# Performance work log

Measured on AMD Instinct MI355X. Metric: run time of the kernel, lower is better.

## Reference

```python
import jax, jax.numpy as jnp
import numpy as np

N_ATOMS = 100_000   # atom_node.size(0)
N_EDGES = 3_200_000  # avg degree 32


def setup_inputs() -> dict:
    key = jax.random.key(0)
    k1, k2, k3, k4, k5 = jax.random.split(key, 5)
    disp = jax.random.normal(k1, (N_EDGES, 3), dtype=jnp.float32)
    a = jax.random.normal(k2, (N_EDGES,), dtype=jnp.float32)
    b = jax.random.normal(k3, (N_EDGES,), dtype=jnp.float32)
    edge_index = jax.random.randint(k4, (2, N_EDGES), 0, N_ATOMS, dtype=jnp.int64)
    atom_node = jax.random.randint(k5, (N_ATOMS,), 0, 100, dtype=jnp.int64)
    return {"disp": disp, "a": a, "b": b, "edge_index": edge_index, "atom_node": atom_node}


def _energy(disp, a, b):
    # surrogate differentiable per-edge energy: E = sum_e a_e*r2_e + b_e*exp(-r2_e)
    r2 = jnp.sum(disp * disp, axis=-1)  # [E]
    return jnp.sum(a * r2 + b * jnp.exp(-r2))


def reference(disp, a, b, edge_index, atom_node):
    n = atom_node.shape[0]
    # force = -dE/d(disp), create_graph analog: jax grads are differentiable
    force_edge = -jax.grad(_energy, argnums=0)(disp, a, b)  # [E,3]
    # dual scatter-add over the two endpoint index rows, then subtract
    f_src = jax.ops.segment_sum(force_edge, edge_index[0], num_segments=n)  # [N,3]
    f_dst = jax.ops.segment_sum(force_edge, edge_index[1], num_segments=n)  # [N,3]
    return f_src - f_dst
```

## Files before the change

kernel.cpp:

```cpp
#include <hip/hip_runtime.h>
#include <hip/hip_bf16.h>
#include <hip/hip_fp16.h>
#include <math.h>
#include <stdint.h>

constexpr int TPB         = 256;
constexpr int U           = 4;
constexpr int ROUND_EDGES = TPB * U;
constexpr int ROUND_REC   = ROUND_EDGES * 2;
constexpr int EPB         = 2048;
constexpr int NPB_SHIFT   = 10;
constexpr int NODES_PER_B = 1 << NPB_SHIFT;
constexpr int NB_MAX      = 128;
constexpr int CAP         = 56;
constexpr int SPLIT       = 8;
constexpr int OCAP        = 262144;

__device__ __forceinline__ uint64_t pack_rec(int local, float fx, float fy, float fz) {
    uint64_t hx = __half_as_ushort(__float2half(fx));
    uint64_t hy = __half_as_ushort(__float2half(fy));
    uint64_t hz = __half_as_ushort(__float2half(fz));
    return (uint64_t)(unsigned)local | (hx << 16) | (hy << 32) | (hz << 48);
}

__global__ void __launch_bounds__(TPB)
p1_partition(const float* __restrict__ disp,
             const float* __restrict__ a,
             const float* __restrict__ b,
             const int* __restrict__ src,
             const int* __restrict__ dst,
             uint64_t* __restrict__ grecords,
             int* __restrict__ gcnt,
             uint4* __restrict__ ovf,
             int* __restrict__ ovf_cnt,
             int E, int NB, int NBLK) {
    __shared__ int      s_cnt[NB_MAX];
    __shared__ int      s_off[NB_MAX];
    __shared__ int      s_gd[NB_MAX];
    __shared__ uint64_t s_rec[ROUND_REC];
    __shared__ uint8_t  s_bin[ROUND_REC];

    const int t = threadIdx.x;
    const int blk = blockIdx.x;
    const int base = blk * EPB;
    const int bend = min(base + EPB, E);

    int wcur = 0;

    for (int rb = base; rb < bend; rb += ROUND_EDGES) {
        const int rend = min(rb + ROUND_EDGES, bend);
        if (t < NB_MAX) s_cnt[t] = 0;
        __syncthreads();

        const int e0 = rb + t * U;
        float dxv[U], dyv[U], dzv[U], av[U], bv[U];
        int sv[U], dv[U];
        bool valid[U];
        if (e0 + U <= rend) {
            const float4* p = (const float4*)(disp + (size_t)3 * e0);
            float4 q0 = p[0], q1 = p[1], q2 = p[2];
            dxv[0] = q0.x; dyv[0] = q0.y; dzv[0] = q0.z;
            dxv[1] = q0.w; dyv[1] = q1.x; dzv[1] = q1.y;
            dxv[2] = q1.z; dyv[2] = q1.w; dzv[2] = q2.x;
            dxv[3] = q2.y; dyv[3] = q2.z; dzv[3] = q2.w;
            float4 qa = *(const float4*)(a + e0);
            av[0] = qa.x; av[1] = qa.y; av[2] = qa.z; av[3] = qa.w;
            float4 qb = *(const float4*)(b + e0);
            bv[0] = qb.x; bv[1] = qb.y; bv[2] = qb.z; bv[3] = qb.w;
            int4 qs = *(const int4*)(src + e0);
            sv[0] = qs.x; sv[1] = qs.y; sv[2] = qs.z; sv[3] = qs.w;
            int4 qd = *(const int4*)(dst + e0);
            dv[0] = qd.x; dv[1] = qd.y; dv[2] = qd.z; dv[3] = qd.w;
#pragma unroll
            for (int u = 0; u < U; ++u) valid[u] = true;
        } else {
#pragma unroll
            for (int u = 0; u < U; ++u) {
                int e = e0 + u;
                valid[u] = (e < rend);
                if (valid[u]) {
                    dxv[u] = disp[3 * e + 0];
                    dyv[u] = disp[3 * e + 1];
                    dzv[u] = disp[3 * e + 2];
                    av[u] = a[e]; bv[u] = b[e];
                    sv[u] = src[e]; dv[u] = dst[e];
                }
            }
        }

        uint64_t rec[2 * U];
        int rbin[2 * U], rrank[2 * U];
#pragma unroll
        for (int u = 0; u < U; ++u) {
            if (valid[u]) {
                float dx = dxv[u], dy = dyv[u], dz = dzv[u];
                float r2 = dx * dx + dy * dy + dz * dz;
                float coef = -2.0f * (av[u] - bv[u] * __expf(-r2));
                float fx = coef * dx, fy = coef * dy, fz = coef * dz;
                int nds[2] = { sv[u], dv[u] };
#pragma unroll
                for (int j = 0; j < 2; ++j) {
                    int k = 2 * u + j;
                    float s = j ? -1.0f : 1.0f;
                    int node = nds[j];
                    rec[k] = pack_rec(node & (NODES_PER_B - 1), s * fx, s * fy, s * fz);
                    rbin[k] = node >> NPB_SHIFT;
                    rrank[k] = atomicAdd(&s_cnt[rbin[k]], 1);
                }
            } else {
                rbin[2 * u] = -1; rbin[2 * u + 1] = -1;
            }
        }
        __syncthreads();

        if (t < 64) {
            int v0 = s_cnt[t];
            int v1 = s_cnt[64 + t];
#pragma unroll
            for (int d = 1; d < 64; d <<= 1) {
                int u0 = __shfl_up(v0, d, 64);
                int u1 = __shfl_up(v1, d, 64);
                if (t >= d) { v0 += u0; v1 += u1; }
            }
            int total0 = __shfl(v0, 63, 64);
            s_off[t] = v0;
            s_off[64 + t] = v1 + total0;
        }
        __syncthreads();

        if (t < NB) {
            int c = s_cnt[t];
            s_gd[t] = wcur - (s_off[t] - c);
            wcur += c;
        }
#pragma unroll
        for (int k = 0; k < 2 * U; ++k) {
            if (rbin[k] >= 0) {
                int pos = s_off[rbin[k]] - s_cnt[rbin[k]] + rrank[k];
                s_rec[pos] = rec[k];
                s_bin[pos] = (uint8_t)rbin[k];
            }
        }
        __syncthreads();

        const int total = s_off[NB_MAX - 1];
        for (int i = t; i < total; i += TPB) {
            uint64_t q = s_rec[i];
            int bin = (int)s_bin[i];
            int pos = s_gd[bin] + i;
            if ((unsigned)pos < (unsigned)CAP) {
                grecords[((size_t)bin * NBLK + blk) * CAP + pos] = q;
            } else {
                int o = atomicAdd(ovf_cnt, 1);
                if (o < OCAP) {
                    uint4 v;
                    v.x = (unsigned)((bin << NPB_SHIFT) | (int)(q & (NODES_PER_B - 1)));
                    v.y = __float_as_uint(__half2float(__ushort_as_half((unsigned short)(q >> 16))));
                    v.z = __float_as_uint(__half2float(__ushort_as_half((unsigned short)(q >> 32))));
                    v.w = __float_as_uint(__half2float(__ushort_as_half((unsigned short)(q >> 48))));
                    ovf[o] = v;
                }
            }
        }
        __syncthreads();
    }

    if (t < NB) gcnt[(size_t)t * NBLK + blk] = min(wcur, CAP);
}

__device__ __forceinline__ uint64_t enc_xyz(float vx, float vy, float vz) {
    vx = fminf(fmaxf(vx, -63.0f), 63.0f);
    vy = fminf(fmaxf(vy, -63.0f), 63.0f);
    vz = fminf(fmaxf(vz, -63.0f), 63.0f);
    unsigned ex = (unsigned)((int)rintf(vx * 64.0f) + 4096);
    unsigned ey = (unsigned)((int)rintf(vy * 64.0f) + 4096);
    unsigned ez = (unsigned)((int)rintf(vz * 64.0f) + 4096);
    return (1ull << 54) | ((uint64_t)ez << 36) | ((uint64_t)ey << 18) | (uint64_t)ex;
}

__global__ void __launch_bounds__(TPB)
p2_reduce(const uint64_t* __restrict__ grecords,
          const int* __restrict__ gcnt,
          float* __restrict__ partials,
          int NB, int NBLK) {
    __shared__ unsigned long long accA[NODES_PER_B];
    const int t = threadIdx.x;
    const int bucket = blockIdx.x >> 3;
    const int part   = blockIdx.x & (SPLIT - 1);

    for (int i = t; i < NODES_PER_B; i += TPB) accA[i] = 0ull;
    __syncthreads();

    const int totslots = NBLK * CAP;
    int lo = (int)((long long)totslots * part / SPLIT);
    int hi = (int)((long long)totslots * (part + 1) / SPLIT);
    const uint64_t* rbase = grecords + (size_t)bucket * totslots;
    const int*      cbase = gcnt     + (size_t)bucket * NBLK;

    int i = lo + t;
    for (; i + 3 * TPB < hi; i += 4 * TPB) {
        bool v[4]; uint64_t q[4];
#pragma unroll
        for (int u = 0; u < 4; ++u) {
            int j = i + u * TPB;
            int nb = j / CAP;
            int slot = j - nb * CAP;
            v[u] = slot < cbase[nb];
            q[u] = v[u] ? rbase[j] : 0ull;
        }
#pragma unroll
        for (int u = 0; u < 4; ++u) {
            if (v[u]) {
                uint64_t q0 = q[u];
                int local = (int)(q0 & (NODES_PER_B - 1));
                float vx = __half2float(__ushort_as_half((unsigned short)(q0 >> 16)));
                float vy = __half2float(__ushort_as_half((unsigned short)(q0 >> 32)));
                float vz = __half2float(__ushort_as_half((unsigned short)(q0 >> 48)));
                atomicAdd(&accA[local], (unsigned long long)enc_xyz(vx, vy, vz));
            }
        }
    }
    for (; i < hi; i += TPB) {
        int nb = i / CAP;
        int slot = i - nb * CAP;
        if (slot < cbase[nb]) {
            uint64_t q0 = rbase[i];
            int local = (int)(q0 & (NODES_PER_B - 1));
            float vx = __half2float(__ushort_as_half((unsigned short)(q0 >> 16)));
            float vy = __half2float(__ushort_as_half((unsigned short)(q0 >> 32)));
            float vz = __half2float(__ushort_as_half((unsigned short)(q0 >> 48)));
            atomicAdd(&accA[local], (unsigned long long)enc_xyz(vx, vy, vz));
        }
    }
    __syncthreads();

    float* pb = partials + (size_t)part * ((size_t)NB * NODES_PER_B * 3)
              + (size_t)bucket * NODES_PER_B * 3;
    for (int k = t; k < NODES_PER_B; k += TPB) {
        uint64_t A = accA[k];
        float cnt = (float)(unsigned)(A >> 54);
        float xf = (float)(int)(A & 0x3FFFFull);
        float yf = (float)(int)((A >> 18) & 0x3FFFFull);
        float zf = (float)(int)((A >> 36) & 0x3FFFFull);
        float bias = cnt * 4096.0f;
        pb[k * 3 + 0] = (xf - bias) * (1.0f / 64.0f);
        pb[k * 3 + 1] = (yf - bias) * (1.0f / 64.0f);
        pb[k * 3 + 2] = (zf - bias) * (1.0f / 64.0f);
    }
}

__global__ void __launch_bounds__(TPB)
p4_sum_partials(const float* __restrict__ partials, float* __restrict__ out,
                int out_size, size_t pstride) {
    int i = blockIdx.x * blockDim.x + threadIdx.x;
    if (i >= out_size) return;
    float s = 0.0f;
#pragma unroll
    for (int p = 0; p < SPLIT; ++p)
        s += partials[(size_t)p * pstride + i];
    out[i] = s;
}

__global__ void __launch_bounds__(TPB)
p3_overflow(const uint4* __restrict__ ovf, const int* __restrict__ ovf_cnt,
            float* __restrict__ out) {
    int n = *ovf_cnt;
    if (n > OCAP) n = OCAP;
    int stride = gridDim.x * blockDim.x;
    for (int i = blockIdx.x * blockDim.x + threadIdx.x; i < n; i += stride) {
        uint4 r = ovf[i];
        int node = (int)r.x;
        unsafeAtomicAdd(&out[node * 3 + 0], __uint_as_float(r.y));
        unsafeAtomicAdd(&out[node * 3 + 1], __uint_as_float(r.z));
        unsafeAtomicAdd(&out[node * 3 + 2], __uint_as_float(r.w));
    }
}

__global__ void __launch_bounds__(TPB)
edge_force_scatter_direct(const float* __restrict__ disp,
                          const float* __restrict__ a,
                          const float* __restrict__ b,
                          const int* __restrict__ src,
                          const int* __restrict__ dst,
                          float* __restrict__ out,
                          int E) {
    int e = blockIdx.x * blockDim.x + threadIdx.x;
    if (e >= E) return;
    float dx = disp[3 * e + 0], dy = disp[3 * e + 1], dz = disp[3 * e + 2];
    float r2 = dx * dx + dy * dy + dz * dz;
    float coef = -2.0f * (a[e] - b[e] * __expf(-r2));
    float fx = coef * dx, fy = coef * dy, fz = coef * dz;
    int s = 3 * src[e], d = 3 * dst[e];
    unsafeAtomicAdd(&out[s + 0], fx);
    unsafeAtomicAdd(&out[s + 1], fy);
    unsafeAtomicAdd(&out[s + 2], fz);
    unsafeAtomicAdd(&out[d + 0], -fx);
    unsafeAtomicAdd(&out[d + 1], -fy);
    unsafeAtomicAdd(&out[d + 2], -fz);
}

extern "C" void kernel_launch(void* const* d_in, const int* in_sizes, int n_in,
                              void* d_out, int out_size, void* d_ws, size_t ws_size,
                              hipStream_t stream) {
    const float* disp = (const float*)d_in[0];
    const float* a    = (const float*)d_in[1];
    const float* b    = (const float*)d_in[2];
    const int*   ei   = (const int*)d_in[3];

    int E = in_sizes[1];
    int N = in_sizes[4];
    float* out = (float*)d_out;

    int NB = (N + NODES_PER_B - 1) >> NPB_SHIFT;
    int NBLK = (E + EPB - 1) / EPB;
    size_t pstride = (size_t)NB * NODES_PER_B * 3;

    size_t gcnt_bytes = (((size_t)NB * NBLK * sizeof(int)) + 255) & ~(size_t)255;
    size_t rec_bytes  = (size_t)NB * NBLK * CAP * sizeof(uint64_t);
    size_t need = 256
                + gcnt_bytes
                + rec_bytes
                + (size_t)OCAP * sizeof(uint4)
                + (size_t)SPLIT * pstride * sizeof(float);

    if (NB <= NB_MAX && ws_size >= need) {
        char* wsb = (char*)d_ws;
        int* ovf_cnt       = (int*)wsb;
        int* gcnt          = (int*)(wsb + 256);
        uint64_t* grecords = (uint64_t*)(wsb + 256 + gcnt_bytes);
        uint4* ovf         = (uint4*)(wsb + 256 + gcnt_bytes + rec_bytes);
        float* partials    = (float*)((char*)ovf + (size_t)OCAP * sizeof(uint4));

        (void)hipMemsetAsync(wsb, 0, 256, stream);

        p1_partition<<<NBLK, TPB, 0, stream>>>(
            disp, a, b, ei, ei + E, grecords, gcnt, ovf, ovf_cnt, E, NB, NBLK);
        p2_reduce<<<NB * SPLIT, TPB, 0, stream>>>(
            grecords, gcnt, partials, NB, NBLK);
        int grid4 = (out_size + TPB - 1) / TPB;
        p4_sum_partials<<<grid4, TPB, 0, stream>>>(partials, out, out_size, pstride);
        p3_overflow<<<64, TPB, 0, stream>>>(ovf, ovf_cnt, out);
    } else {
        (void)hipMemsetAsync(d_out, 0, (size_t)out_size * sizeof(float), stream);
        int grid = (E + TPB - 1) / TPB;
        edge_force_scatter_direct<<<grid, TPB, 0, stream>>>(
            disp, a, b, ei, ei + E, out, E);
    }
}
```

Before: 186.8 us.

## Drop per-segment count array; zero-pad record segments and single-round partition

The partition kernel now handles one round of 2048 edges per block with 8 edges per thread, replacing the multi-round loop and its running write cursor. Instead of writing a per-bin count array, each block zero-fills the unused tail of every record segment, and the reduce kernel skips records equal to zero. This removes the count loads and the divide/modulo per slot in the reduce kernel and lets it unroll 8-wide. The cost is extra zero-fill stores for empty slots, and a valid record that packs to exactly zero (local node 0 with a zero force) is treated as empty, which is harmless because it adds nothing.

```diff
diff --git a/kernel.cpp b/kernel.cpp
--- a/kernel.cpp
+++ b/kernel.cpp
@@ -5,10 +5,9 @@
 #include <stdint.h>
 
 constexpr int TPB         = 256;
-constexpr int U           = 4;
-constexpr int ROUND_EDGES = TPB * U;
-constexpr int ROUND_REC   = ROUND_EDGES * 2;
-constexpr int EPB         = 2048;
+constexpr int U           = 8;
+constexpr int EPB         = TPB * U;
+constexpr int RECS        = EPB * 2;
 constexpr int NPB_SHIFT   = 10;
 constexpr int NODES_PER_B = 1 << NPB_SHIFT;
 constexpr int NB_MAX      = 128;
@@ -30,142 +29,152 @@
              const int* __restrict__ src,
              const int* __restrict__ dst,
              uint64_t* __restrict__ grecords,
-             int* __restrict__ gcnt,
              uint4* __restrict__ ovf,
              int* __restrict__ ovf_cnt,
              int E, int NB, int NBLK) {
     __shared__ int      s_cnt[NB_MAX];
     __shared__ int      s_off[NB_MAX];
     __shared__ int      s_gd[NB_MAX];
-    __shared__ uint64_t s_rec[ROUND_REC];
-    __shared__ uint8_t  s_bin[ROUND_REC];
+    __shared__ uint64_t s_rec[RECS];
+    __shared__ uint8_t  s_bin[RECS];
 
     const int t = threadIdx.x;
     const int blk = blockIdx.x;
     const int base = blk * EPB;
     const int bend = min(base + EPB, E);
 
-    int wcur = 0;
-
-    for (int rb = base; rb < bend; rb += ROUND_EDGES) {
-        const int rend = min(rb + ROUND_EDGES, bend);
-        if (t < NB_MAX) s_cnt[t] = 0;
-        __syncthreads();
-
-        const int e0 = rb + t * U;
-        float dxv[U], dyv[U], dzv[U], av[U], bv[U];
-        int sv[U], dv[U];
-        bool valid[U];
-        if (e0 + U <= rend) {
-            const float4* p = (const float4*)(disp + (size_t)3 * e0);
-            float4 q0 = p[0], q1 = p[1], q2 = p[2];
-            dxv[0] = q0.x; dyv[0] = q0.y; dzv[0] = q0.z;
-            dxv[1] = q0.w; dyv[1] = q1.x; dzv[1] = q1.y;
-            dxv[2] = q1.z; dyv[2] = q1.w; dzv[2] = q2.x;
-            dxv[3] = q2.y; dyv[3] = q2.z; dzv[3] = q2.w;
-            float4 qa = *(const float4*)(a + e0);
-            av[0] = qa.x; av[1] = qa.y; av[2] = qa.z; av[3] = qa.w;
-            float4 qb = *(const float4*)(b + e0);
-            bv[0] = qb.x; bv[1] = qb.y; bv[2] = qb.z; bv[3] = qb.w;
-            int4 qs = *(const int4*)(src + e0);
-            sv[0] = qs.x; sv[1] = qs.y; sv[2] = qs.z; sv[3] = qs.w;
-            int4 qd = *(const int4*)(dst + e0);
-            dv[0] = qd.x; dv[1] = qd.y; dv[2] = qd.z; dv[3] = qd.w;
-#pragma unroll
-            for (int u = 0; u < U; ++u) valid[u] = true;
+    if (t < NB_MAX) s_cnt[t] = 0;
+    __syncthreads();
+
+    const int e0 = base + t * U;
+    float dxv[U], dyv[U], dzv[U], av[U], bv[U];
+    int sv[U], dv[U];
+    bool valid[U];
+    if (e0 + U <= bend) {
+        const float4* p = (const float4*)(disp + (size_t)3 * e0);
+        float4 q0 = p[0], q1 = p[1], q2 = p[2];
+        float4 q3 = p[3], q4 = p[4], q5 = p[5];
+        dxv[0] = q0.x; dyv[0] = q0.y; dzv[0] = q0.z;
+        dxv[1] = q0.w; dyv[1] = q1.x; dzv[1] = q1.y;
+        dxv[2] = q1.z; dyv[2] = q1.w; dzv[2] = q2.x;
+        dxv[3] = q2.y; dyv[3] = q2.z; dzv[3] = q2.w;
+        dxv[4] = q3.x; dyv[4] = q3.y; dzv[4] = q3.z;
+        dxv[5] = q3.w; dyv[5] = q4.x; dzv[5] = q4.y;
+        dxv[6] = q4.z; dyv[6] = q4.w; dzv[6] = q5.x;
+        dxv[7] = q5.y; dyv[7] = q5.z; dzv[7] = q5.w;
+        float4 qa0 = *(const float4*)(a + e0);
+        float4 qa1 = *(const float4*)(a + e0 + 4);
+        av[0] = qa0.x; av[1] = qa0.y; av[2] = qa0.z; av[3] = qa0.w;
+        av[4] = qa1.x; av[5] = qa1.y; av[6] = qa1.z; av[7] = qa1.w;
+        float4 qb0 = *(const float4*)(b + e0);
+        float4 qb1 = *(const float4*)(b + e0 + 4);
+        bv[0] = qb0.x; bv[1] = qb0.y; bv[2] = qb0.z; bv[3] = qb0.w;
+        bv[4] = qb1.x; bv[5] = qb1.y; bv[6] = qb1.z; bv[7] = qb1.w;
+        int4 qs0 = *(const int4*)(src + e0);
+        int4 qs1 = *(const int4*)(src + e0 + 4);
+        sv[0] = qs0.x; sv[1] = qs0.y; sv[2] = qs0.z; sv[3] = qs0.w;
+        sv[4] = qs1.x; sv[5] = qs1.y; sv[6] = qs1.z; sv[7] = qs1.w;
+        int4 qd0 = *(const int4*)(dst + e0);
+        int4 qd1 = *(const int4*)(dst + e0 + 4);
+        dv[0] = qd0.x; dv[1] = qd0.y; dv[2] = qd0.z; dv[3] = qd0.w;
+        dv[4] = qd1.x; dv[5] = qd1.y; dv[6] = qd1.z; dv[7] = qd1.w;
+#pragma unroll
+        for (int u = 0; u < U; ++u) valid[u] = true;
+    } else {
+#pragma unroll
+        for (int u = 0; u < U; ++u) {
+            int e = e0 + u;
+            valid[u] = (e < bend);
+            if (valid[u]) {
+                dxv[u] = disp[3 * e + 0];
+                dyv[u] = disp[3 * e + 1];
+                dzv[u] = disp[3 * e + 2];
+                av[u] = a[e]; bv[u] = b[e];
+                sv[u] = src[e]; dv[u] = dst[e];
+            }
+        }
+    }
+
+    uint64_t rec[2 * U];
+    int meta[2 * U];
+#pragma unroll
+    for (int u = 0; u < U; ++u) {
+        if (valid[u]) {
+            float dx = dxv[u], dy = dyv[u], dz = dzv[u];
+            float r2 = dx * dx + dy * dy + dz * dz;
+            float coef = -2.0f * (av[u] - bv[u] * __expf(-r2));
+            float fx = coef * dx, fy = coef * dy, fz = coef * dz;
+            int nds[2] = { sv[u], dv[u] };
+#pragma unroll
+            for (int j = 0; j < 2; ++j) {
+                int k = 2 * u + j;
+                float s = j ? -1.0f : 1.0f;
+                int node = nds[j];
+                rec[k] = pack_rec(node & (NODES_PER_B - 1), s * fx, s * fy, s * fz);
+                int bin = node >> NPB_SHIFT;
+                int rank = atomicAdd(&s_cnt[bin], 1);
+                meta[k] = (bin << 16) | rank;
+            }
         } else {
-#pragma unroll
-            for (int u = 0; u < U; ++u) {
-                int e = e0 + u;
-                valid[u] = (e < rend);
-                if (valid[u]) {
-                    dxv[u] = disp[3 * e + 0];
-                    dyv[u] = disp[3 * e + 1];
-                    dzv[u] = disp[3 * e + 2];
-                    av[u] = a[e]; bv[u] = b[e];
-                    sv[u] = src[e]; dv[u] = dst[e];
-                }
+            meta[2 * u] = -1; meta[2 * u + 1] = -1;
+        }
+    }
+    __syncthreads();
+
+    if (t < 64) {
+        int v0 = s_cnt[t];
+        int v1 = s_cnt[64 + t];
+#pragma unroll
+        for (int d = 1; d < 64; d <<= 1) {
+            int u0 = __shfl_up(v0, d, 64);
+            int u1 = __shfl_up(v1, d, 64);
+            if (t >= d) { v0 += u0; v1 += u1; }
+        }
+        int total0 = __shfl(v0, 63, 64);
+        s_off[t] = v0;
+        s_off[64 + t] = v1 + total0;
+    }
+    __syncthreads();
+
+    if (t < NB) {
+        s_gd[t] = s_cnt[t] - s_off[t];
+    }
+#pragma unroll
+    for (int k = 0; k < 2 * U; ++k) {
+        if (meta[k] >= 0) {
+            int bin = meta[k] >> 16;
+            int rank = meta[k] & 0xFFFF;
+            int pos = s_off[bin] - s_cnt[bin] + rank;
+            s_rec[pos] = rec[k];
+            s_bin[pos] = (uint8_t)bin;
+        }
+    }
+    __syncthreads();
+
+    if (t < NB) {
+        uint64_t* seg = grecords + ((size_t)t * NBLK + blk) * CAP;
+        for (int p = s_cnt[t]; p < CAP; ++p) seg[p] = 0ull;
+    }
+
+    const int total = s_off[NB_MAX - 1];
+    for (int i = t; i < total; i += TPB) {
+        uint64_t q = s_rec[i];
+        int bin = (int)s_bin[i];
+        int pos = s_gd[bin] + i;
+        if ((unsigned)pos < (unsigned)CAP) {
+            grecords[((size_t)bin * NBLK + blk) * CAP + pos] = q;
+        } else {
+            int o = atomicAdd(ovf_cnt, 1);
+            if (o < OCAP) {
+                uint4 v;
+                v.x = (unsigned)((bin << NPB_SHIFT) | (int)(q & (NODES_PER_B - 1)));
+                v.y = __float_as_uint(__half2float(__ushort_as_half((unsigned short)(q >> 16))));
+                v.z = __float_as_uint(__half2float(__ushort_as_half((unsigned short)(q >> 32))));
+                v.w = __float_as_uint(__half2float(__ushort_as_half((unsigned short)(q >> 48))));
+                ovf[o] = v;
             }
         }
-
-        uint64_t rec[2 * U];
-        int rbin[2 * U], rrank[2 * U];
-#pragma unroll
-        for (int u = 0; u < U; ++u) {
-            if (valid[u]) {
-                float dx = dxv[u], dy = dyv[u], dz = dzv[u];
-                float r2 = dx * dx + dy * dy + dz * dz;
-                float coef = -2.0f * (av[u] - bv[u] * __expf(-r2));
-                float fx = coef * dx, fy = coef * dy, fz = coef * dz;
-                int nds[2] = { sv[u], dv[u] };
-#pragma unroll
-                for (int j = 0; j < 2; ++j) {
-                    int k = 2 * u + j;
-                    float s = j ? -1.0f : 1.0f;
-                    int node = nds[j];
-                    rec[k] = pack_rec(node & (NODES_PER_B - 1), s * fx, s * fy, s * fz);
-                    rbin[k] = node >> NPB_SHIFT;
-                    rrank[k] = atomicAdd(&s_cnt[rbin[k]], 1);
-                }
-            } else {
-                rbin[2 * u] = -1; rbin[2 * u + 1] = -1;
-            }
-        }
-        __syncthreads();
-
-        if (t < 64) {
-            int v0 = s_cnt[t];
-            int v1 = s_cnt[64 + t];
-#pragma unroll
-            for (int d = 1; d < 64; d <<= 1) {
-                int u0 = __shfl_up(v0, d, 64);
-                int u1 = __shfl_up(v1, d, 64);
-                if (t >= d) { v0 += u0; v1 += u1; }
-            }
-            int total0 = __shfl(v0, 63, 64);
-            s_off[t] = v0;
-            s_off[64 + t] = v1 + total0;
-        }
-        __syncthreads();
-
-        if (t < NB) {
-            int c = s_cnt[t];
-            s_gd[t] = wcur - (s_off[t] - c);
-            wcur += c;
-        }
-#pragma unroll
-        for (int k = 0; k < 2 * U; ++k) {
-            if (rbin[k] >= 0) {
-                int pos = s_off[rbin[k]] - s_cnt[rbin[k]] + rrank[k];
-                s_rec[pos] = rec[k];
-                s_bin[pos] = (uint8_t)rbin[k];
-            }
-        }
-        __syncthreads();
-
-        const int total = s_off[NB_MAX - 1];
-        for (int i = t; i < total; i += TPB) {
-            uint64_t q = s_rec[i];
-            int bin = (int)s_bin[i];
-            int pos = s_gd[bin] + i;
-            if ((unsigned)pos < (unsigned)CAP) {
-                grecords[((size_t)bin * NBLK + blk) * CAP + pos] = q;
-            } else {
-                int o = atomicAdd(ovf_cnt, 1);
-                if (o < OCAP) {
-                    uint4 v;
-                    v.x = (unsigned)((bin << NPB_SHIFT) | (int)(q & (NODES_PER_B - 1)));
-                    v.y = __float_as_uint(__half2float(__ushort_as_half((unsigned short)(q >> 16))));
-                    v.z = __float_as_uint(__half2float(__ushort_as_half((unsigned short)(q >> 32))));
-                    v.w = __float_as_uint(__half2float(__ushort_as_half((unsigned short)(q >> 48))));
-                    ovf[o] = v;
-                }
-            }
-        }
-        __syncthreads();
-    }
-
-    if (t < NB) gcnt[(size_t)t * NBLK + blk] = min(wcur, CAP);
+    }
 }
 
 __device__ __forceinline__ uint64_t enc_xyz(float vx, float vy, float vz) {
@@ -180,7 +189,6 @@
 
 __global__ void __launch_bounds__(TPB)
 p2_reduce(const uint64_t* __restrict__ grecords,
-          const int* __restrict__ gcnt,
           float* __restrict__ partials,
           int NB, int NBLK) {
     __shared__ unsigned long long accA[NODES_PER_B];
@@ -195,23 +203,16 @@
     int lo = (int)((long long)totslots * part / SPLIT);
     int hi = (int)((long long)totslots * (part + 1) / SPLIT);
     const uint64_t* rbase = grecords + (size_t)bucket * totslots;
-    const int*      cbase = gcnt     + (size_t)bucket * NBLK;
 
     int i = lo + t;
-    for (; i + 3 * TPB < hi; i += 4 * TPB) {
-        bool v[4]; uint64_t q[4];
-#pragma unroll
-        for (int u = 0; u < 4; ++u) {
-            int j = i + u * TPB;
-            int nb = j / CAP;
-            int slot = j - nb * CAP;
-            v[u] = slot < cbase[nb];
-            q[u] = v[u] ? rbase[j] : 0ull;
-        }
-#pragma unroll
-        for (int u = 0; u < 4; ++u) {
-            if (v[u]) {
-                uint64_t q0 = q[u];
+    for (; i + 7 * TPB < hi; i += 8 * TPB) {
+        uint64_t q[8];
+#pragma unroll
+        for (int u = 0; u < 8; ++u) q[u] = rbase[i + u * TPB];
+#pragma unroll
+        for (int u = 0; u < 8; ++u) {
+            uint64_t q0 = q[u];
+            if (q0 != 0ull) {
                 int local = (int)(q0 & (NODES_PER_B - 1));
                 float vx = __half2float(__ushort_as_half((unsigned short)(q0 >> 16)));
                 float vy = __half2float(__ushort_as_half((unsigned short)(q0 >> 32)));
@@ -221,10 +222,8 @@
         }
     }
     for (; i < hi; i += TPB) {
-        int nb = i / CAP;
-        int slot = i - nb * CAP;
-        if (slot < cbase[nb]) {
-            uint64_t q0 = rbase[i];
+        uint64_t q0 = rbase[i];
+        if (q0 != 0ull) {
             int local = (int)(q0 & (NODES_PER_B - 1));
             float vx = __half2float(__ushort_as_half((unsigned short)(q0 >> 16)));
             float vy = __half2float(__ushort_as_half((unsigned short)(q0 >> 32)));
@@ -315,10 +314,8 @@
     int NBLK = (E + EPB - 1) / EPB;
     size_t pstride = (size_t)NB * NODES_PER_B * 3;
 
-    size_t gcnt_bytes = (((size_t)NB * NBLK * sizeof(int)) + 255) & ~(size_t)255;
     size_t rec_bytes  = (size_t)NB * NBLK * CAP * sizeof(uint64_t);
     size_t need = 256
-                + gcnt_bytes
                 + rec_bytes
                 + (size_t)OCAP * sizeof(uint4)
                 + (size_t)SPLIT * pstride * sizeof(float);
@@ -326,17 +323,16 @@
     if (NB <= NB_MAX && ws_size >= need) {
         char* wsb = (char*)d_ws;
         int* ovf_cnt       = (int*)wsb;
-        int* gcnt          = (int*)(wsb + 256);
-        uint64_t* grecords = (uint64_t*)(wsb + 256 + gcnt_bytes);
-        uint4* ovf         = (uint4*)(wsb + 256 + gcnt_bytes + rec_bytes);
+        uint64_t* grecords = (uint64_t*)(wsb + 256);
+        uint4* ovf         = (uint4*)(wsb + 256 + rec_bytes);
         float* partials    = (float*)((char*)ovf + (size_t)OCAP * sizeof(uint4));
 
         (void)hipMemsetAsync(wsb, 0, 256, stream);
 
         p1_partition<<<NBLK, TPB, 0, stream>>>(
-            disp, a, b, ei, ei + E, grecords, gcnt, ovf, ovf_cnt, E, NB, NBLK);
+            disp, a, b, ei, ei + E, grecords, ovf, ovf_cnt, E, NB, NBLK);
         p2_reduce<<<NB * SPLIT, TPB, 0, stream>>>(
-            grecords, gcnt, partials, NB, NBLK);
+            grecords, partials, NB, NBLK);
         int grid4 = (out_size + TPB - 1) / TPB;
         p4_sum_partials<<<grid4, TPB, 0, stream>>>(partials, out, out_size, pstride);
         p3_overflow<<<64, TPB, 0, stream>>>(ovf, ovf_cnt, out);
```

Result: faster. 166.2 us (median of 2 runs) (-11.0%).
